# Kernel optimization log

Hardware: AMD Instinct MI355X
Metric: run time of the kernel (lower is better)

The kernel has to match this reference:

```python
import jax, jax.numpy as jnp
import numpy as np

N_NODES = 50000
N_EDGES = 640000
IN_FEAT = 128
EDGE_FEAT = 256
EDGE_EMBED = 32
OUT_CLASSES = 2


def setup_inputs() -> dict:
    key = jax.random.key(0)
    ks = jax.random.split(key, 8)
    h = jax.random.normal(ks[0], (N_NODES, IN_FEAT), dtype=jnp.float32)
    src = jax.random.randint(ks[1], (N_EDGES,), 0, N_NODES)
    dst = jax.random.randint(ks[2], (N_EDGES,), 0, N_NODES)
    e = jax.random.normal(ks[3], (N_EDGES, EDGE_EMBED), dtype=jnp.float32)
    # Linear weights stored torch-style: [out, in]
    W1_w = jax.random.normal(ks[4], (EDGE_FEAT, 2 * IN_FEAT), dtype=jnp.float32) * (1.0 / np.sqrt(2 * IN_FEAT))
    W1_b = jax.random.normal(ks[5], (EDGE_FEAT,), dtype=jnp.float32) * 0.01
    W2_w = jax.random.normal(ks[6], (OUT_CLASSES, EDGE_FEAT + EDGE_EMBED), dtype=jnp.float32) * (1.0 / np.sqrt(EDGE_FEAT + EDGE_EMBED))
    W2_b = jax.random.normal(ks[7], (OUT_CLASSES,), dtype=jnp.float32) * 0.01
    return {"h": h, "src": src, "dst": dst, "e": e,
            "W1_w": W1_w, "W1_b": W1_b, "W2_w": W2_w, "W2_b": W2_b}


def reference(h, src, dst, e, W1_w, W1_b, W2_w, W2_b):
    # Edge-wise gather of endpoint features
    h_u = h[src]                       # [E, F]
    h_v = h[dst]                       # [E, F]
    h_uv = jnp.concatenate([h_u, h_v], axis=1)        # [E, 2F]
    h_e = h_uv @ W1_w.T + W1_b                         # [E, edge_features]
    he_e = jnp.concatenate([h_e, e], axis=1)           # [E, edge_features + edge_embed]
    score = he_e @ W2_w.T + W2_b                       # [E, out_classes]
    return score
```

## Files before the change

### kernel.cpp

```cpp
#include <hip/hip_runtime.h>

#define IN_FEAT    128
#define EDGE_EMBED 32

__global__ __launch_bounds__(256) void precompute_kernel(
    const float* __restrict__ W1_w, const float* __restrict__ W1_b,
    const float* __restrict__ W2_w, const float* __restrict__ W2_b,
    float* __restrict__ ws) {
    const int f = threadIdx.x;
    float m0 = 0.f, m1 = 0.f;
#pragma unroll 16
    for (int k = 0; k < 256; ++k) {
        const float w1 = W1_w[k * 256 + f];
        m0 = fmaf(w1, W2_w[k], m0);
        m1 = fmaf(w1, W2_w[288 + k], m1);
    }
    ws[f * 2 + 0] = m0;
    ws[f * 2 + 1] = m1;

    if (threadIdx.x < 64) {
        const int t = threadIdx.x;
        float b0 = 0.f, b1 = 0.f;
#pragma unroll
        for (int m = 0; m < 4; ++m) {
            const int k = t + 64 * m;
            const float wb = W1_b[k];
            b0 = fmaf(wb, W2_w[k], b0);
            b1 = fmaf(wb, W2_w[288 + k], b1);
        }
#pragma unroll
        for (int m = 32; m >= 1; m >>= 1) {
            b0 += __shfl_xor(b0, m);
            b1 += __shfl_xor(b1, m);
        }
        if (t == 0) {
            ws[512] = b0 + W2_b[0];
            ws[513] = b1 + W2_b[1];
        }
    }
}

__global__ __launch_bounds__(256, 8) void node_proj_kernel(
    const float* __restrict__ h, const float* __restrict__ ws,
    float* __restrict__ pu, float* __restrict__ pv, int N) {
    const int p = threadIdx.x & 31;
    const int node = blockIdx.x * 8 + (threadIdx.x >> 5);
    if (node >= N) return;

    const float4 muA = *(const float4*)(ws + p * 8);
    const float4 muB = *(const float4*)(ws + p * 8 + 4);
    const float4 mvA = *(const float4*)(ws + 256 + p * 8);
    const float4 mvB = *(const float4*)(ws + 256 + p * 8 + 4);

    const float4 hr = *(const float4*)(h + (size_t)node * IN_FEAT + p * 4);

    float u0 = hr.x * muA.x, u1 = hr.x * muA.y;
    u0 = fmaf(hr.y, muA.z, u0); u1 = fmaf(hr.y, muA.w, u1);
    u0 = fmaf(hr.z, muB.x, u0); u1 = fmaf(hr.z, muB.y, u1);
    u0 = fmaf(hr.w, muB.z, u0); u1 = fmaf(hr.w, muB.w, u1);
    float v0 = hr.x * mvA.x, v1 = hr.x * mvA.y;
    v0 = fmaf(hr.y, mvA.z, v0); v1 = fmaf(hr.y, mvA.w, v1);
    v0 = fmaf(hr.z, mvB.x, v0); v1 = fmaf(hr.z, mvB.y, v1);
    v0 = fmaf(hr.w, mvB.z, v0); v1 = fmaf(hr.w, mvB.w, v1);

#pragma unroll
    for (int m = 16; m >= 1; m >>= 1) {
        u0 += __shfl_xor(u0, m); u1 += __shfl_xor(u1, m);
        v0 += __shfl_xor(v0, m); v1 += __shfl_xor(v1, m);
    }
    if (p == 0) {
        *(float2*)(pu + (size_t)node * 2) = make_float2(u0, u1);
        *(float2*)(pv + (size_t)node * 2) = make_float2(v0, v1);
    }
}

__global__ __launch_bounds__(256, 8) void edge_score_kernel(
    const int* __restrict__ src, const int* __restrict__ dst,
    const float* __restrict__ e, const float* __restrict__ W2_w,
    const float* __restrict__ ws, const float* __restrict__ pu,
    const float* __restrict__ pv, float* __restrict__ out,
    int E, int numGroups) {
    const int p = threadIdx.x & 7;
    int group = blockIdx.x * (blockDim.x >> 3) + (threadIdx.x >> 3);

    const float4 w0 = *(const float4*)(W2_w + 256 + p * 4);
    const float4 w1 = *(const float4*)(W2_w + 544 + p * 4);
    const float b0 = ws[512], b1 = ws[513];

    for (int edge = group; edge < E; edge += numGroups) {
        const float4 ev = *(const float4*)(e + (size_t)edge * EDGE_EMBED + p * 4);

        float acc0 = ev.x * w0.x;
        float acc1 = ev.x * w1.x;
        acc0 = fmaf(ev.y, w0.y, acc0); acc1 = fmaf(ev.y, w1.y, acc1);
        acc0 = fmaf(ev.z, w0.z, acc0); acc1 = fmaf(ev.z, w1.z, acc1);
        acc0 = fmaf(ev.w, w0.w, acc0); acc1 = fmaf(ev.w, w1.w, acc1);

        if (p == 0) {
            const int s = src[edge];
            const float2 u = *(const float2*)(pu + (size_t)s * 2);
            acc0 += u.x; acc1 += u.y;
        } else if (p == 4) {
            const int d = dst[edge];
            const float2 v = *(const float2*)(pv + (size_t)d * 2);
            acc0 += v.x; acc1 += v.y;
        }

#pragma unroll
        for (int m = 4; m >= 1; m >>= 1) {
            acc0 += __shfl_xor(acc0, m);
            acc1 += __shfl_xor(acc1, m);
        }
        if (p == 0) {
            *(float2*)(out + (size_t)edge * 2) = make_float2(acc0 + b0, acc1 + b1);
        }
    }
}

extern "C" void kernel_launch(void* const* d_in, const int* in_sizes, int n_in,
                              void* d_out, int out_size, void* d_ws, size_t ws_size,
                              hipStream_t stream) {
    const float* h    = (const float*)d_in[0];
    const int*   src  = (const int*)d_in[1];
    const int*   dst  = (const int*)d_in[2];
    const float* e    = (const float*)d_in[3];
    const float* W1_w = (const float*)d_in[4];
    const float* W1_b = (const float*)d_in[5];
    const float* W2_w = (const float*)d_in[6];
    const float* W2_b = (const float*)d_in[7];
    float* out = (float*)d_out;
    float* ws  = (float*)d_ws;

    const int E = in_sizes[1];
    const int N = in_sizes[0] / IN_FEAT;

    float* pu = ws + 1024;
    float* pv = ws + 1024 + (size_t)N * 2;

    precompute_kernel<<<1, 256, 0, stream>>>(W1_w, W1_b, W2_w, W2_b, ws);
    node_proj_kernel<<<(N + 7) / 8, 256, 0, stream>>>(h, ws, pu, pv, N);

    const int BLOCKS = 2048;
    const int numGroups = BLOCKS * (256 / 8);
    edge_score_kernel<<<BLOCKS, 256, 0, stream>>>(src, dst, e, W2_w, ws, pu, pv,
                                                  out, E, numGroups);
}
```

Before: 171.8 us.

## Use one thread per edge and split precompute reduction across 1024 threads

The edge kernel now assigns one thread per edge instead of eight lanes per edge. Each thread reads the full 32-float embedding row, both gathered node projections and writes the output directly, which removes the shuffle reduction and the grid-stride loop. The single-block precompute kernel now spreads the K loop over four 256-thread chunks and combines the partial sums in shared memory, shortening the serial chain. The per-thread edge access is strided by 128 bytes across lanes, so the e loads become uncoalesced, though each thread consumes whole cache lines.

```diff
diff --git a/kernel.cpp b/kernel.cpp
--- a/kernel.cpp
+++ b/kernel.cpp
@@ -3,21 +3,28 @@
 #define IN_FEAT    128
 #define EDGE_EMBED 32
 
-__global__ __launch_bounds__(256) void precompute_kernel(
+__global__ __launch_bounds__(1024) void precompute_kernel(
     const float* __restrict__ W1_w, const float* __restrict__ W1_b,
     const float* __restrict__ W2_w, const float* __restrict__ W2_b,
     float* __restrict__ ws) {
-    const int f = threadIdx.x;
+    __shared__ float part[4][512];
+    const int f = threadIdx.x & 255;
+    const int chunk = threadIdx.x >> 8;
     float m0 = 0.f, m1 = 0.f;
 #pragma unroll 16
-    for (int k = 0; k < 256; ++k) {
+    for (int kk = 0; kk < 64; ++kk) {
+        const int k = chunk * 64 + kk;
         const float w1 = W1_w[k * 256 + f];
         m0 = fmaf(w1, W2_w[k], m0);
         m1 = fmaf(w1, W2_w[288 + k], m1);
     }
-    ws[f * 2 + 0] = m0;
-    ws[f * 2 + 1] = m1;
-
+    part[chunk][f * 2 + 0] = m0;
+    part[chunk][f * 2 + 1] = m1;
+    __syncthreads();
+    if (chunk == 0) {
+        ws[f * 2 + 0] = part[0][f * 2] + part[1][f * 2] + part[2][f * 2] + part[3][f * 2];
+        ws[f * 2 + 1] = part[0][f * 2 + 1] + part[1][f * 2 + 1] + part[2][f * 2 + 1] + part[3][f * 2 + 1];
+    }
     if (threadIdx.x < 64) {
         const int t = threadIdx.x;
         float b0 = 0.f, b1 = 0.f;
@@ -74,47 +81,34 @@
     }
 }
 
-__global__ __launch_bounds__(256, 8) void edge_score_kernel(
+__global__ __launch_bounds__(256, 4) void edge_score_kernel(
     const int* __restrict__ src, const int* __restrict__ dst,
     const float* __restrict__ e, const float* __restrict__ W2_w,
     const float* __restrict__ ws, const float* __restrict__ pu,
-    const float* __restrict__ pv, float* __restrict__ out,
-    int E, int numGroups) {
-    const int p = threadIdx.x & 7;
-    int group = blockIdx.x * (blockDim.x >> 3) + (threadIdx.x >> 3);
+    const float* __restrict__ pv, float* __restrict__ out, int E) {
+    const int i = blockIdx.x * blockDim.x + threadIdx.x;
+    if (i >= E) return;
 
-    const float4 w0 = *(const float4*)(W2_w + 256 + p * 4);
-    const float4 w1 = *(const float4*)(W2_w + 544 + p * 4);
-    const float b0 = ws[512], b1 = ws[513];
+    const int s = src[i];
+    const int d = dst[i];
+    const float2 u = *(const float2*)(pu + (size_t)s * 2);
+    const float2 v = *(const float2*)(pv + (size_t)d * 2);
 
-    for (int edge = group; edge < E; edge += numGroups) {
-        const float4 ev = *(const float4*)(e + (size_t)edge * EDGE_EMBED + p * 4);
+    float acc0 = u.x + v.x + ws[512];
+    float acc1 = u.y + v.y + ws[513];
 
-        float acc0 = ev.x * w0.x;
-        float acc1 = ev.x * w1.x;
-        acc0 = fmaf(ev.y, w0.y, acc0); acc1 = fmaf(ev.y, w1.y, acc1);
-        acc0 = fmaf(ev.z, w0.z, acc0); acc1 = fmaf(ev.z, w1.z, acc1);
-        acc0 = fmaf(ev.w, w0.w, acc0); acc1 = fmaf(ev.w, w1.w, acc1);
-
-        if (p == 0) {
-            const int s = src[edge];
-            const float2 u = *(const float2*)(pu + (size_t)s * 2);
-            acc0 += u.x; acc1 += u.y;
-        } else if (p == 4) {
-            const int d = dst[edge];
-            const float2 v = *(const float2*)(pv + (size_t)d * 2);
-            acc0 += v.x; acc1 += v.y;
-        }
-
+    const float* ep = e + (size_t)i * EDGE_EMBED;
 #pragma unroll
-        for (int m = 4; m >= 1; m >>= 1) {
-            acc0 += __shfl_xor(acc0, m);
-            acc1 += __shfl_xor(acc1, m);
-        }
-        if (p == 0) {
-            *(float2*)(out + (size_t)edge * 2) = make_float2(acc0 + b0, acc1 + b1);
-        }
+    for (int c4 = 0; c4 < 8; ++c4) {
+        const float4 ev = *(const float4*)(ep + c4 * 4);
+        const float4 wa = *(const float4*)(W2_w + 256 + c4 * 4);
+        const float4 wb = *(const float4*)(W2_w + 544 + c4 * 4);
+        acc0 = fmaf(ev.x, wa.x, acc0); acc1 = fmaf(ev.x, wb.x, acc1);
+        acc0 = fmaf(ev.y, wa.y, acc0); acc1 = fmaf(ev.y, wb.y, acc1);
+        acc0 = fmaf(ev.z, wa.z, acc0); acc1 = fmaf(ev.z, wb.z, acc1);
+        acc0 = fmaf(ev.w, wa.w, acc0); acc1 = fmaf(ev.w, wb.w, acc1);
     }
+    *(float2*)(out + (size_t)i * 2) = make_float2(acc0, acc1);
 }
 
 extern "C" void kernel_launch(void* const* d_in, const int* in_sizes, int n_in,
@@ -137,11 +131,8 @@
     float* pu = ws + 1024;
     float* pv = ws + 1024 + (size_t)N * 2;
 
-    precompute_kernel<<<1, 256, 0, stream>>>(W1_w, W1_b, W2_w, W2_b, ws);
+    precompute_kernel<<<1, 1024, 0, stream>>>(W1_w, W1_b, W2_w, W2_b, ws);
     node_proj_kernel<<<(N + 7) / 8, 256, 0, stream>>>(h, ws, pu, pv, N);
-
-    const int BLOCKS = 2048;
-    const int numGroups = BLOCKS * (256 / 8);
-    edge_score_kernel<<<BLOCKS, 256, 0, stream>>>(src, dst, e, W2_w, ws, pu, pv,
-                                                  out, E, numGroups);
+    edge_score_kernel<<<(E + 255) / 256, 256, 0, stream>>>(src, dst, e, W2_w, ws,
+                                                           pu, pv, out, E);
 }
```

New measurement: 172.7 us. No clear change (+0.5%).
